# Kernel tuning notes

Hardware: AMD Instinct MI355X
Metric: run time of the kernel (lower is better)

Reference implementation:

```python
import jax, jax.numpy as jnp
import numpy as np


def _resize_axis(x, axis, n_out):
    # trilinear (per-axis linear) resize, matching torch align_corners=False
    n_in = x.shape[axis]
    coords = jnp.clip((jnp.arange(n_out) + 0.5) * (n_in / n_out) - 0.5, 0.0, n_in - 1)
    lo = jnp.floor(coords).astype(jnp.int32)
    hi = jnp.minimum(lo + 1, n_in - 1)
    w = (coords - lo).astype(x.dtype)
    shp = [1] * x.ndim
    shp[axis] = n_out
    w = w.reshape(shp)
    return jnp.take(x, lo, axis=axis) * (1 - w) + jnp.take(x, hi, axis=axis) * w


def setup_inputs() -> dict:
    key = jax.random.key(0)
    ks = jax.random.split(key, 16)
    M, B, C, H, W, Z = 4, 1, 64, 64, 64, 64
    mini = max(C // 32, 4)  # = 4
    s = 0.05
    return {
        'modalities': jax.random.normal(ks[0], (M, B, C, H, W, Z), jnp.float32),
        'wq1': jax.random.normal(ks[1], (mini, C), jnp.float32) * s,
        'bq1': jax.random.normal(ks[2], (mini,), jnp.float32) * s,
        'wq2': jax.random.normal(ks[3], (2, mini), jnp.float32) * s,
        'bq2': jax.random.normal(ks[4], (2,), jnp.float32) * s,
        'wa1': jax.random.normal(ks[5], (mini, C), jnp.float32) * s,
        'ba1': jax.random.normal(ks[6], (mini,), jnp.float32) * s,
        'wa2': jax.random.normal(ks[7], (1, mini), jnp.float32) * s,
        'ba2': jax.random.normal(ks[8], (1,), jnp.float32) * s,
        'wf': jax.random.normal(ks[9], (C, C), jnp.float32) * s,
        'bf': jax.random.normal(ks[10], (C,), jnp.float32) * s,
        'wg1': jax.random.normal(ks[11], (mini, C), jnp.float32) * s,
        'bg1': jax.random.normal(ks[12], (mini,), jnp.float32) * s,
        'wg2': jax.random.normal(ks[13], (C, mini), jnp.float32) * s,
        'bg2': jax.random.normal(ks[14], (C,), jnp.float32) * s,
    }


def reference(modalities, wq1, bq1, wq2, bq2, wa1, ba1, wa2, ba2, wf, bf, wg1, bg1, wg2, bg2):
    M, B, C, H, W, Z = modalities.shape
    x = modalities
    # quality net: GAP -> 1x1 conv -> relu -> 1x1 conv -> sigmoid (all 1x1x1 convs == matmuls)
    gap = x.mean(axis=(3, 4, 5))  # [M,B,C]
    scores = jax.nn.sigmoid(jnp.maximum(gap @ wq1.T + bq1, 0.0) @ wq2.T + bq2)  # [M,B,2]
    qw = scores.mean(axis=2)      # quality_weight per modality, [M,B] (mean over ch+unit spatial)
    t = qw.mean(axis=1)           # scalar weight contribution per modality, [M]
    # cross attention: adaptive avg pool to 4^3, tiny MLP, trilinear upsample back to H,W,Z
    d = x.reshape(M, B, C, 4, H // 4, 4, W // 4, 4, Z // 4).mean(axis=(4, 6, 8))  # [M,B,C,4,4,4]
    h = jnp.maximum(jnp.einsum('mbcxyz,kc->mbkxyz', d, wa1) + ba1.reshape(1, 1, -1, 1, 1, 1), 0.0)
    a = jax.nn.sigmoid(jnp.einsum('mbkxyz,ok->mboxyz', h, wa2) + ba2.reshape(1, 1, -1, 1, 1, 1))
    a = _resize_axis(_resize_axis(_resize_axis(a, 3, H), 4, W), 5, Z)  # [M,B,1,H,W,Z]
    # pairwise aggregation: enhancement_i = sum_{j!=i} x_j * attn_j * qw_j, normalized by sum_{j!=i} t_j
    contrib = x * a * qw[:, :, None, None, None, None]  # [M,B,C,H,W,Z]
    S = contrib.sum(axis=0, keepdims=True)
    T = t.sum()
    enh = (S - contrib) / (T - t)[:, None, None, None, None, None]
    # fusion 1x1 conv + gate
    fused = jnp.einsum('mbchwz,dc->mbdhwz', enh, wf) + bf.reshape(1, 1, -1, 1, 1, 1)
    g = fused.mean(axis=(3, 4, 5))  # [M,B,C]
    gate = jax.nn.sigmoid(jnp.maximum(g @ wg1.T + bg1, 0.0) @ wg2.T + bg2)  # [M,B,C]
    enhanced = x + gate[:, :, :, None, None, None] * fused
    boundary = scores[:, :, 0].reshape(M, B, 1, 1, 1, 1)
    semantic = scores[:, :, 1].reshape(M, B, 1, 1, 1, 1)
    return enhanced, boundary, semantic
```

## Files before the change

### kernel.cpp

```cpp
#include <hip/hip_runtime.h>
#include <math.h>

typedef __attribute__((ext_vector_type(4))) float f4;
typedef __attribute__((ext_vector_type(8))) short s8v;
typedef __attribute__((ext_vector_type(4))) unsigned int u4v;
typedef __attribute__((ext_vector_type(2))) unsigned int u2v;

#define NVOX 262144
#define MB_TOT 67108864

__device__ __forceinline__ float sigm(float x){ return 1.0f/(1.0f+expf(-x)); }
__device__ __forceinline__ unsigned short f2b(float f){
  unsigned x = __float_as_uint(f);
  return (unsigned short)((x + 0x7fffu + ((x>>16)&1u)) >> 16);
}
__device__ __forceinline__ unsigned cvtpk(float lo, float hi){
  unsigned r;
  asm("v_cvt_pk_bf16_f32 %0, %1, %2" : "=v"(r) : "v"(lo), "v"(hi));
  return r;
}
__device__ __forceinline__ float bl(unsigned u){ return __uint_as_float(u<<16); }
__device__ __forceinline__ float bh(unsigned u){ return __uint_as_float(u & 0xffff0000u); }

__global__ __launch_bounds__(1024) void k_pass1(const float* __restrict__ x,
                                                float* __restrict__ dsums,
                                                float* __restrict__ xbsums){
  __shared__ float rowdat[8][1024];
  __shared__ float txb[64][16];
  __shared__ float tbs[64][16];
  int tid = threadIdx.x;
  int mc = blockIdx.x;
  const float* xp = x + (size_t)mc * NVOX;
  int chunk = tid & 15;
  int rbase = tid >> 4;
  float wq0,wq1,wq2,wq3; int lzc;
  {
    int z0 = chunk*4;
    float cz = fminf(fmaxf((z0+0.5f)*0.0625f-0.5f, 0.0f), 3.0f);
    lzc = (int)cz;
    wq0 = cz - (float)lzc;
    cz = fminf(fmaxf((z0+1.5f)*0.0625f-0.5f, 0.0f), 3.0f); wq1 = cz - (float)lzc;
    cz = fminf(fmaxf((z0+2.5f)*0.0625f-0.5f, 0.0f), 3.0f); wq2 = cz - (float)lzc;
    cz = fminf(fmaxf((z0+3.5f)*0.0625f-0.5f, 0.0f), 3.0f); wq3 = cz - (float)lzc;
  }
  int kb = chunk >> 2;
  for (int round=0; round<4; ++round){
#pragma unroll
    for (int itg=0; itg<4; ++itg){
      f4 u[4];
#pragma unroll
      for (int s=0;s<4;++s){
        int it = itg*4+s;
        int row = round*1024 + it*64 + rbase;
        u[s] = *reinterpret_cast<const f4*>(xp + (size_t)row*64 + chunk*4);
      }
#pragma unroll
      for (int s=0;s<4;++s){
        int it = itg*4+s;
        int rir = it*64 + rbase;
        f4 v = u[s];
        float ksP = (v.x+v.y)+(v.z+v.w);
        float wB = v.x*wq0 + v.y*wq1 + v.z*wq2 + v.w*wq3;
        float wA = ksP - wB;
        ksP += __shfl_xor(ksP, 1, 64);
        ksP += __shfl_xor(ksP, 2, 64);
        float w0 = (lzc==0)?wA:0.f;
        float w1 = (lzc==1)?wA:((lzc==0)?wB:0.f);
        float w2 = (lzc==2)?wA:((lzc==1)?wB:0.f);
        float w3 = (lzc==3)?wA:((lzc==2)?wB:0.f);
#pragma unroll
        for (int mk=1; mk<16; mk<<=1){
          w0 += __shfl_xor(w0, mk, 64);
          w1 += __shfl_xor(w1, mk, 64);
          w2 += __shfl_xor(w2, mk, 64);
          w3 += __shfl_xor(w3, mk, 64);
        }
        if ((chunk&3)==0) rowdat[kb][rir] = ksP;
        if (chunk==0) rowdat[4][rir]=w0;
        if (chunk==1) rowdat[5][rir]=w1;
        if (chunk==2) rowdat[6][rir]=w2;
        if (chunk==3) rowdat[7][rir]=w3;
      }
    }
    __syncthreads();
    if (tid < 256){
      int il = tid>>4, py=(tid>>2)&3, pz=tid&3;
      int base = il*64;
      float s=0.f;
      for (int jj=0; jj<64; ++jj){
        int j = (jj + tid) & 63;
        float cj = fminf(fmaxf((j+0.5f)*0.0625f-0.5f, 0.0f), 3.0f);
        int lj=(int)cj; float wj=cj-(float)lj;
        float w = (py==lj)?(1.f-wj):((py==lj+1)?wj:0.f);
        s += w * rowdat[4+pz][base+j];
      }
      txb[round*16+il][py*4+pz] = s;
    } else if (tid < 512){
      int u2 = tid-256;
      int il = u2>>4, jq=(u2>>2)&3, kq=u2&3;
      int base = il*64 + jq*16;
      float s=0.f;
      for (int jj=0; jj<16; ++jj) s += rowdat[kq][base + ((jj+u2)&15)];
      tbs[round*16+il][jq*4+kq] = s;
    }
    __syncthreads();
  }
  if (tid < 64){
    int px = tid>>4, py=(tid>>2)&3, pz=tid&3;
    float s=0.f;
    for (int i=0;i<64;++i){
      float ci = fminf(fmaxf((i+0.5f)*0.0625f-0.5f, 0.0f), 3.0f);
      int li=(int)ci; float wi=ci-(float)li;
      float w = (px==li)?(1.f-wi):((px==li+1)?wi:0.f);
      s += w * txb[i][py*4+pz];
    }
    xbsums[(size_t)mc*64+tid] = s;
  } else if (tid < 128){
    int p = tid-64;
    int iq = p>>4, jq=(p>>2)&3, kq=p&3;
    float s=0.f;
    for (int i=iq*16; i<iq*16+16; ++i) s += tbs[i][jq*4+kq];
    dsums[(size_t)mc*64+p] = s;
  }
}

__global__ __launch_bounds__(256) void k_pass2(
    const float* __restrict__ dsums, const float* __restrict__ xbsums,
    const float* __restrict__ wq1, const float* __restrict__ bq1,
    const float* __restrict__ wq2, const float* __restrict__ bq2,
    const float* __restrict__ wa1, const float* __restrict__ ba1,
    const float* __restrict__ wa2, const float* __restrict__ ba2,
    const float* __restrict__ wf,  const float* __restrict__ bfv,
    const float* __restrict__ wg1, const float* __restrict__ bg1,
    const float* __restrict__ wg2, const float* __restrict__ bg2,
    float* __restrict__ wsa, float* __restrict__ wsgate,
    float* __restrict__ wsqw, float* __restrict__ wsinv,
    unsigned short* __restrict__ wfb,
    float* __restrict__ outp)
{
  __shared__ float sGap[256];
  __shared__ float sA[256];
  __shared__ float sCm[256];
  __shared__ float sG[256];
  __shared__ float sGG[16];
  __shared__ float sQw[4];
  int tid = threadIdx.x;
  int m = tid>>6, c = tid&63;
  for (int t = tid; t < 4096; t += 256) wfb[t] = f2b(wf[t]);
  {
    float s=0.f;
    const float* dp = dsums + (size_t)tid*64;
    for (int p=0;p<64;++p) s += dp[p];
    sGap[tid] = s * (1.0f/262144.0f);
  }
  {
    int p = c;
    float h0=0,h1=0,h2=0,h3=0;
    for (int cc=0; cc<64; ++cc){
      float dm = dsums[((size_t)(m*64+cc))*64+p] * (1.0f/4096.0f);
      h0 += dm * wa1[0*64+cc];
      h1 += dm * wa1[1*64+cc];
      h2 += dm * wa1[2*64+cc];
      h3 += dm * wa1[3*64+cc];
    }
    h0 = fmaxf(h0 + ba1[0], 0.f);
    h1 = fmaxf(h1 + ba1[1], 0.f);
    h2 = fmaxf(h2 + ba1[2], 0.f);
    h3 = fmaxf(h3 + ba1[3], 0.f);
    float s = h0*wa2[0] + h1*wa2[1] + h2*wa2[2] + h3*wa2[3] + ba2[0];
    float aa = sigm(s);
    sA[tid] = aa;
    wsa[tid] = aa;
  }
  __syncthreads();
  if (tid < 4){
    int mm = tid;
    float q0=0,q1=0,q2=0,q3=0;
    for (int cc=0; cc<64; ++cc){
      float g = sGap[mm*64+cc];
      q0 += g*wq1[0*64+cc];
      q1 += g*wq1[1*64+cc];
      q2 += g*wq1[2*64+cc];
      q3 += g*wq1[3*64+cc];
    }
    q0 = fmaxf(q0+bq1[0],0.f); q1 = fmaxf(q1+bq1[1],0.f);
    q2 = fmaxf(q2+bq1[2],0.f); q3 = fmaxf(q3+bq1[3],0.f);
    float s0 = sigm(q0*wq2[0]+q1*wq2[1]+q2*wq2[2]+q3*wq2[3]+bq2[0]);
    float s1 = sigm(q0*wq2[4]+q1*wq2[5]+q2*wq2[6]+q3*wq2[7]+bq2[1]);
    sQw[mm] = 0.5f*(s0+s1);
    outp[MB_TOT + mm]     = s0;
    outp[MB_TOT + 4 + mm] = s1;
  }
  __syncthreads();
  float qw_m = sQw[m];
  float T = sQw[0]+sQw[1]+sQw[2]+sQw[3];
  float inv_m = 1.0f/(T - qw_m);
  if (tid < 4){ wsqw[tid] = sQw[tid]; wsinv[tid] = 1.0f/(T - sQw[tid]); }
  {
    const float* xbp = xbsums + (size_t)tid*64;
    float s=0.f;
    for (int p=0;p<64;++p) s += sA[m*64+p]*xbp[p];
    sCm[tid] = qw_m * s * (1.0f/262144.0f);
  }
  __syncthreads();
  {
    int dd = c;
    float acc=0.f;
    for (int cc=0; cc<64; ++cc){
      float Sm = sCm[0*64+cc]+sCm[1*64+cc]+sCm[2*64+cc]+sCm[3*64+cc];
      float em = (Sm - sCm[m*64+cc]) * inv_m;
      acc += em * wf[dd*64+cc];
    }
    sG[tid] = acc + bfv[dd];
  }
  __syncthreads();
  if (tid < 16){
    int mm = tid>>2, k = tid&3;
    float acc=0.f;
    for (int dd=0; dd<64; ++dd) acc += sG[mm*64+dd]*wg1[k*64+dd];
    sGG[tid] = fmaxf(acc + bg1[k], 0.f);
  }
  __syncthreads();
  {
    float s = sGG[m*4+0]*wg2[c*4+0] + sGG[m*4+1]*wg2[c*4+1]
            + sGG[m*4+2]*wg2[c*4+2] + sGG[m*4+3]*wg2[c*4+3] + bg2[c];
    wsgate[tid] = sigm(s);
  }
}

__global__ __launch_bounds__(256) void k_pass3(
    const float* __restrict__ x, const unsigned short* __restrict__ wfb,
    const float* __restrict__ bfv,
    const float* __restrict__ wsa, const float* __restrict__ wsgate,
    const float* __restrict__ wsqw, const float* __restrict__ wsinv,
    float* __restrict__ outp)
{
  __shared__ unsigned int xt[4][32][66];
  __shared__ unsigned int fusedT[64][34];
  __shared__ float aCell[4][64];
  __shared__ float gateL[4][64];
  __shared__ __align__(16) float auq[4][64];
  __shared__ float bfL[64];
  __shared__ float A2[4][4];
  int tid = threadIdx.x;
  int b = blockIdx.x;
  int i = b >> 6, j = b & 63;
  size_t V0 = (size_t)b * 64;
  int w    = tid >> 6;
  int lane = tid & 63;
  int ks   = lane >> 4;
  int r    = lane & 15;
  int vox16 = w << 4;

  const float* xw = x + (size_t)(w*64)*NVOX + V0 + r*4;
  f4 v[16];
#pragma unroll
  for (int rr=0; rr<16; ++rr){
    int cc = ks*16 + rr;
    v[rr] = *reinterpret_cast<const f4*>(xw + (size_t)cc*NVOX);
  }
  aCell[w][lane] = wsa[tid];
  gateL[w][lane] = wsgate[tid];
  if (tid < 64) bfL[tid] = bfv[tid];
#pragma unroll
  for (int rr=0; rr<16; rr+=2){
    u4v pk;
#pragma unroll
    for (int q=0;q<4;++q) pk[q] = cvtpk(v[rr][q], v[rr+1][q]);
    *reinterpret_cast<u4v*>(&xt[w][ks*8 + (rr>>1)][r*4]) = pk;
  }
  __syncthreads();

  if (tid < 16){
    int mm = tid>>2, pz = tid&3;
    float ci = fminf(fmaxf((i+0.5f)*0.0625f-0.5f,0.f),3.f);
    int li=(int)ci; float wi=ci-(float)li; int hiI=li<3?li+1:3;
    float cj = fminf(fmaxf((j+0.5f)*0.0625f-0.5f,0.f),3.f);
    int lj=(int)cj; float wj=cj-(float)lj; int hj=lj<3?lj+1:3;
    A2[mm][pz] = (1.f-wi)*((1.f-wj)*aCell[mm][li*16+lj*4+pz] + wj*aCell[mm][li*16+hj*4+pz])
               + wi*((1.f-wj)*aCell[mm][hiI*16+lj*4+pz] + wj*aCell[mm][hiI*16+hj*4+pz]);
  }
  __syncthreads();
  {
    int mm = tid>>6, z = tid&63;
    float cz = fminf(fmaxf((z+0.5f)*0.0625f-0.5f,0.f),3.f);
    int lz=(int)cz; float wzf=cz-(float)lz; int hz=lz<3?lz+1:3;
    auq[mm][z] = ((1.f-wzf)*A2[mm][lz] + wzf*A2[mm][hz]) * wsqw[mm];
  }
  __syncthreads();

  s8v bfr[4][2];
#pragma unroll
  for (int t=0;t<4;++t)
#pragma unroll
    for (int kk=0;kk<2;++kk)
      bfr[t][kk] = *reinterpret_cast<const s8v*>(&wfb[(t*16 + r)*64 + kk*32 + ks*8]);

  f4 acc[4][4];
#pragma unroll
  for (int mm=0;mm<4;++mm)
#pragma unroll
    for (int t=0;t<4;++t) acc[mm][t] = f4{0.f,0.f,0.f,0.f};

#pragma unroll
  for (int mm=0;mm<4;++mm){
    union { unsigned int u[4]; s8v s; } A0, A1;
#pragma unroll
    for (int q=0;q<4;++q){
      A0.u[q] = xt[mm][ks*4+q][vox16+r];
      A1.u[q] = xt[mm][16+ks*4+q][vox16+r];
    }
#pragma unroll
    for (int t=0;t<4;++t){
      acc[mm][t] = __builtin_amdgcn_mfma_f32_16x16x32_bf16(A0.s, bfr[t][0], acc[mm][t], 0,0,0);
      acc[mm][t] = __builtin_amdgcn_mfma_f32_16x16x32_bf16(A1.s, bfr[t][1], acc[mm][t], 0,0,0);
    }
  }

  f4 aq[4]; float invv[4];
#pragma unroll
  for (int mm=0;mm<4;++mm){
    aq[mm]  = *reinterpret_cast<const f4*>(&auq[mm][vox16 + 4*ks]);
    invv[mm] = wsinv[mm];
  }
  f4 FS[4];
#pragma unroll
  for (int t=0;t<4;++t){
    FS[t] = f4{0.f,0.f,0.f,0.f};
#pragma unroll
    for (int mm=0;mm<4;++mm)
#pragma unroll
      for (int q=0;q<4;++q) FS[t][q] += aq[mm][q]*acc[mm][t][q];
  }

  int g4 = tid >> 4;
  int r4l = tid & 15;
#pragma unroll
  for (int mm=0;mm<4;++mm){
#pragma unroll
    for (int t=0;t<4;++t){
      int dd = t*16 + r;
      float bfvv = bfL[dd];
      float f0 = (FS[t][0] - aq[mm][0]*acc[mm][t][0])*invv[mm] + bfvv;
      float f1 = (FS[t][1] - aq[mm][1]*acc[mm][t][1])*invv[mm] + bfvv;
      float f2 = (FS[t][2] - aq[mm][2]*acc[mm][t][2])*invv[mm] + bfvv;
      float f3 = (FS[t][3] - aq[mm][3]*acc[mm][t][3])*invv[mm] + bfvv;
      u2v pk2;
      pk2.x = cvtpk(f0, f1);
      pk2.y = cvtpk(f2, f3);
      *reinterpret_cast<u2v*>(&fusedT[dd][(vox16 + ks*4)>>1]) = pk2;
    }
    __syncthreads();
#pragma unroll
    for (int rr=0; rr<4; ++rr){
      int dd = rr*16 + g4;
      float g = gateL[mm][dd];
      u4v xu = *reinterpret_cast<const u4v*>(&xt[mm][dd>>1][r4l*4]);
      u2v fu = *reinterpret_cast<const u2v*>(&fusedT[dd][r4l*2]);
      f4 o;
      float x0 = (dd&1) ? bh(xu[0]) : bl(xu[0]);
      float x1 = (dd&1) ? bh(xu[1]) : bl(xu[1]);
      float x2 = (dd&1) ? bh(xu[2]) : bl(xu[2]);
      float x3 = (dd&1) ? bh(xu[3]) : bl(xu[3]);
      o[0] = x0 + g*bl(fu.x);
      o[1] = x1 + g*bh(fu.x);
      o[2] = x2 + g*bl(fu.y);
      o[3] = x3 + g*bh(fu.y);
      *reinterpret_cast<f4*>(outp + (size_t)(mm*64+dd)*NVOX + V0 + r4l*4) = o;
    }
    __syncthreads();
  }
}

extern "C" void kernel_launch(void* const* d_in, const int* in_sizes, int n_in,
                              void* d_out, int out_size, void* d_ws, size_t ws_size,
                              hipStream_t stream){
  const float* x   = (const float*)d_in[0];
  const float* wq1 = (const float*)d_in[1];
  const float* bq1 = (const float*)d_in[2];
  const float* wq2 = (const float*)d_in[3];
  const float* bq2 = (const float*)d_in[4];
  const float* wa1 = (const float*)d_in[5];
  const float* ba1 = (const float*)d_in[6];
  const float* wa2 = (const float*)d_in[7];
  const float* ba2 = (const float*)d_in[8];
  const float* wf  = (const float*)d_in[9];
  const float* bfv = (const float*)d_in[10];
  const float* wg1 = (const float*)d_in[11];
  const float* bg1 = (const float*)d_in[12];
  const float* wg2 = (const float*)d_in[13];
  const float* bg2 = (const float*)d_in[14];
  float* outp = (float*)d_out;
  float* w = (float*)d_ws;
  float* dsums  = w;
  float* xbsums = w + 16384;
  float* wsa    = w + 32768;
  float* wsgate = w + 33024;
  float* wsqw   = w + 33280;
  float* wsinv  = w + 33284;
  unsigned short* wfb = (unsigned short*)(w + 33288);
  hipLaunchKernelGGL(k_pass1, dim3(256), dim3(1024), 0, stream, x, dsums, xbsums);
  hipLaunchKernelGGL(k_pass2, dim3(1), dim3(256), 0, stream, dsums, xbsums,
                     wq1,bq1,wq2,bq2,wa1,ba1,wa2,ba2,wf,bfv,wg1,bg1,wg2,bg2,
                     wsa, wsgate, wsqw, wsinv, wfb, outp);
  hipLaunchKernelGGL(k_pass3, dim3(4096), dim3(256), 0, stream, x, wfb, bfv,
                     wsa, wsgate, wsqw, wsinv, outp);
}
```

Baseline: 212.8 us.

## Restructure pass1 reduction into per-thread register accumulators with LDS atomics

Rewrites the first-pass reduction so each thread owns one (j, z-chunk) column and walks all 64 i rows, accumulating the downsampled sums and the trilinear-weighted sums in registers. A few LDS atomics per thread then replace the staged row buffers, the wide shuffle reductions and the multiple sync rounds. It also pads the transposed LDS tile in pass3 and reverses that kernel's block order, probably to get L2 reuse from data pass1 just read. Trade-offs are higher register pressure from the fully unrolled 64-iteration loop, and atomic contention on the 64 shared bins.

```diff
diff --git a/kernel.cpp b/kernel.cpp
--- a/kernel.cpp
+++ b/kernel.cpp
@@ -22,105 +22,76 @@
 __device__ __forceinline__ float bl(unsigned u){ return __uint_as_float(u<<16); }
 __device__ __forceinline__ float bh(unsigned u){ return __uint_as_float(u & 0xffff0000u); }
 
-__global__ __launch_bounds__(1024) void k_pass1(const float* __restrict__ x,
-                                                float* __restrict__ dsums,
-                                                float* __restrict__ xbsums){
-  __shared__ float rowdat[8][1024];
-  __shared__ float txb[64][16];
-  __shared__ float tbs[64][16];
+__global__ __launch_bounds__(1024, 4) void k_pass1(const float* __restrict__ x,
+                                                   float* __restrict__ dsums,
+                                                   float* __restrict__ xbsums){
+  __shared__ float xbL[64];
+  __shared__ float bsL[64];
   int tid = threadIdx.x;
   int mc = blockIdx.x;
+  if (tid < 64){ xbL[tid]=0.f; bsL[tid]=0.f; }
   const float* xp = x + (size_t)mc * NVOX;
   int chunk = tid & 15;
-  int rbase = tid >> 4;
-  float wq0,wq1,wq2,wq3; int lzc;
-  {
-    int z0 = chunk*4;
-    float cz = fminf(fmaxf((z0+0.5f)*0.0625f-0.5f, 0.0f), 3.0f);
-    lzc = (int)cz;
-    wq0 = cz - (float)lzc;
-    cz = fminf(fmaxf((z0+1.5f)*0.0625f-0.5f, 0.0f), 3.0f); wq1 = cz - (float)lzc;
-    cz = fminf(fmaxf((z0+2.5f)*0.0625f-0.5f, 0.0f), 3.0f); wq2 = cz - (float)lzc;
-    cz = fminf(fmaxf((z0+3.5f)*0.0625f-0.5f, 0.0f), 3.0f); wq3 = cz - (float)lzc;
-  }
-  int kb = chunk >> 2;
-  for (int round=0; round<4; ++round){
-#pragma unroll
-    for (int itg=0; itg<4; ++itg){
-      f4 u[4];
-#pragma unroll
-      for (int s=0;s<4;++s){
-        int it = itg*4+s;
-        int row = round*1024 + it*64 + rbase;
-        u[s] = *reinterpret_cast<const f4*>(xp + (size_t)row*64 + chunk*4);
-      }
-#pragma unroll
-      for (int s=0;s<4;++s){
-        int it = itg*4+s;
-        int rir = it*64 + rbase;
-        f4 v = u[s];
-        float ksP = (v.x+v.y)+(v.z+v.w);
-        float wB = v.x*wq0 + v.y*wq1 + v.z*wq2 + v.w*wq3;
-        float wA = ksP - wB;
-        ksP += __shfl_xor(ksP, 1, 64);
-        ksP += __shfl_xor(ksP, 2, 64);
-        float w0 = (lzc==0)?wA:0.f;
-        float w1 = (lzc==1)?wA:((lzc==0)?wB:0.f);
-        float w2 = (lzc==2)?wA:((lzc==1)?wB:0.f);
-        float w3 = (lzc==3)?wA:((lzc==2)?wB:0.f);
-#pragma unroll
-        for (int mk=1; mk<16; mk<<=1){
-          w0 += __shfl_xor(w0, mk, 64);
-          w1 += __shfl_xor(w1, mk, 64);
-          w2 += __shfl_xor(w2, mk, 64);
-          w3 += __shfl_xor(w3, mk, 64);
-        }
-        if ((chunk&3)==0) rowdat[kb][rir] = ksP;
-        if (chunk==0) rowdat[4][rir]=w0;
-        if (chunk==1) rowdat[5][rir]=w1;
-        if (chunk==2) rowdat[6][rir]=w2;
-        if (chunk==3) rowdat[7][rir]=w3;
-      }
-    }
-    __syncthreads();
-    if (tid < 256){
-      int il = tid>>4, py=(tid>>2)&3, pz=tid&3;
-      int base = il*64;
-      float s=0.f;
-      for (int jj=0; jj<64; ++jj){
-        int j = (jj + tid) & 63;
-        float cj = fminf(fmaxf((j+0.5f)*0.0625f-0.5f, 0.0f), 3.0f);
-        int lj=(int)cj; float wj=cj-(float)lj;
-        float w = (py==lj)?(1.f-wj):((py==lj+1)?wj:0.f);
-        s += w * rowdat[4+pz][base+j];
-      }
-      txb[round*16+il][py*4+pz] = s;
-    } else if (tid < 512){
-      int u2 = tid-256;
-      int il = u2>>4, jq=(u2>>2)&3, kq=u2&3;
-      int base = il*64 + jq*16;
-      float s=0.f;
-      for (int jj=0; jj<16; ++jj) s += rowdat[kq][base + ((jj+u2)&15)];
-      tbs[round*16+il][jq*4+kq] = s;
-    }
-    __syncthreads();
-  }
+  int j     = tid >> 4;
+  float wqz0,wqz1,wqz2,wqz3; int lzc;
+  {
+    float cz = fminf(fmaxf((chunk*4+0.5f)*0.0625f-0.5f, 0.0f), 3.0f);
+    lzc = (int)cz;  wqz0 = cz - (float)lzc;
+    cz = fminf(fmaxf((chunk*4+1.5f)*0.0625f-0.5f, 0.0f), 3.0f); wqz1 = cz - (float)lzc;
+    cz = fminf(fmaxf((chunk*4+2.5f)*0.0625f-0.5f, 0.0f), 3.0f); wqz2 = cz - (float)lzc;
+    cz = fminf(fmaxf((chunk*4+3.5f)*0.0625f-0.5f, 0.0f), 3.0f); wqz3 = cz - (float)lzc;
+  }
+  float cjA, cjB; int lj;
+  {
+    float cj = fminf(fmaxf((j+0.5f)*0.0625f-0.5f, 0.0f), 3.0f);
+    lj = (int)cj; float wj = cj - (float)lj;
+    cjA = 1.0f - wj; cjB = wj;
+  }
+  int jq = j >> 4, kq = chunk >> 2;
+
+  float accx[4][2][2];
+#pragma unroll
+  for (int a=0;a<4;++a){ accx[a][0][0]=0.f; accx[a][0][1]=0.f; accx[a][1][0]=0.f; accx[a][1][1]=0.f; }
+  float accb0=0.f, accb1=0.f, accb2=0.f, accb3=0.f;
+
+#pragma unroll
+  for (int i=0; i<64; ++i){
+    f4 v = *reinterpret_cast<const f4*>(xp + (size_t)(i*64 + j)*64 + chunk*4);
+    float s  = (v.x+v.y)+(v.z+v.w);
+    float wB = v.x*wqz0 + v.y*wqz1 + v.z*wqz2 + v.w*wqz3;
+    float wA = s - wB;
+    if ((i>>4)==0) accb0 += s; else if ((i>>4)==1) accb1 += s;
+    else if ((i>>4)==2) accb2 += s; else accb3 += s;
+    float ci = fminf(fmaxf((i+0.5f)*0.0625f-0.5f, 0.0f), 3.0f);
+    int li = (int)ci; float wi = ci - (float)li;
+    {
+      float pA = 1.0f - wi;
+      float e0 = pA*wA, e1 = pA*wB;
+      accx[li][0][0] += cjA*e0;  accx[li][0][1] += cjA*e1;
+      accx[li][1][0] += cjB*e0;  accx[li][1][1] += cjB*e1;
+    }
+    if (wi > 0.0f){
+      float f0 = wi*wA, f1 = wi*wB;
+      accx[li+1][0][0] += cjA*f0;  accx[li+1][0][1] += cjA*f1;
+      accx[li+1][1][0] += cjB*f0;  accx[li+1][1][1] += cjB*f1;
+    }
+  }
+  __syncthreads();
+#pragma unroll
+  for (int px=0; px<4; ++px){
+    atomicAdd(&xbL[px*16 + lj*4 + lzc], accx[px][0][0]);
+    if (lzc < 3) atomicAdd(&xbL[px*16 + lj*4 + lzc+1], accx[px][0][1]);
+    if (lj  < 3) atomicAdd(&xbL[px*16 + (lj+1)*4 + lzc], accx[px][1][0]);
+    if (lj < 3 && lzc < 3) atomicAdd(&xbL[px*16 + (lj+1)*4 + lzc+1], accx[px][1][1]);
+  }
+  atomicAdd(&bsL[0*16 + jq*4 + kq], accb0);
+  atomicAdd(&bsL[1*16 + jq*4 + kq], accb1);
+  atomicAdd(&bsL[2*16 + jq*4 + kq], accb2);
+  atomicAdd(&bsL[3*16 + jq*4 + kq], accb3);
+  __syncthreads();
   if (tid < 64){
-    int px = tid>>4, py=(tid>>2)&3, pz=tid&3;
-    float s=0.f;
-    for (int i=0;i<64;++i){
-      float ci = fminf(fmaxf((i+0.5f)*0.0625f-0.5f, 0.0f), 3.0f);
-      int li=(int)ci; float wi=ci-(float)li;
-      float w = (px==li)?(1.f-wi):((px==li+1)?wi:0.f);
-      s += w * txb[i][py*4+pz];
-    }
-    xbsums[(size_t)mc*64+tid] = s;
-  } else if (tid < 128){
-    int p = tid-64;
-    int iq = p>>4, jq=(p>>2)&3, kq=p&3;
-    float s=0.f;
-    for (int i=iq*16; i<iq*16+16; ++i) s += tbs[i][jq*4+kq];
-    dsums[(size_t)mc*64+p] = s;
+    xbsums[(size_t)mc*64 + tid] = xbL[tid];
+    dsums [(size_t)mc*64 + tid] = bsL[tid];
   }
 }
 
@@ -235,7 +206,7 @@
     const float* __restrict__ wsqw, const float* __restrict__ wsinv,
     float* __restrict__ outp)
 {
-  __shared__ unsigned int xt[4][32][66];
+  __shared__ unsigned int xt[4][32][68];
   __shared__ unsigned int fusedT[64][34];
   __shared__ float aCell[4][64];
   __shared__ float gateL[4][64];
@@ -243,7 +214,7 @@
   __shared__ float bfL[64];
   __shared__ float A2[4][4];
   int tid = threadIdx.x;
-  int b = blockIdx.x;
+  int b = 4095 - (int)blockIdx.x;
   int i = b >> 6, j = b & 63;
   size_t V0 = (size_t)b * 64;
   int w    = tid >> 6;
```

Result: slower. 299.3 us (+40.6%).

## Split pass1 blocks in half with atomic accumulation and reverse pass3 block order

Applied to the files above, without the earlier changes.

Pass1 now launches two blocks per (modality, channel), each covering half the rows, and accumulates partial pooled sums into workspace with atomicAdd after a memset clears it. This doubles the block count so the 256-CU GPU is better filled during the bandwidth-bound reduction. Pass3 walks its blocks in reverse order, probably so data pass1 touched last is still in cache when pass3 starts, and pads the xt shared array. The cost is an extra memset launch and atomics, and floating-point summation order is no longer deterministic.

```diff
diff --git a/kernel.cpp b/kernel.cpp
--- a/kernel.cpp
+++ b/kernel.cpp
@@ -26,25 +26,26 @@
                                                 float* __restrict__ dsums,
                                                 float* __restrict__ xbsums){
   __shared__ float rowdat[8][1024];
-  __shared__ float txb[64][16];
-  __shared__ float tbs[64][16];
+  __shared__ float txb[32][16];
+  __shared__ float tbs[32][16];
   int tid = threadIdx.x;
-  int mc = blockIdx.x;
+  int b = blockIdx.x;
+  int mc   = b >> 1;
+  int half = b & 1;
   const float* xp = x + (size_t)mc * NVOX;
   int chunk = tid & 15;
   int rbase = tid >> 4;
   float wq0,wq1,wq2,wq3; int lzc;
   {
-    int z0 = chunk*4;
-    float cz = fminf(fmaxf((z0+0.5f)*0.0625f-0.5f, 0.0f), 3.0f);
-    lzc = (int)cz;
-    wq0 = cz - (float)lzc;
-    cz = fminf(fmaxf((z0+1.5f)*0.0625f-0.5f, 0.0f), 3.0f); wq1 = cz - (float)lzc;
-    cz = fminf(fmaxf((z0+2.5f)*0.0625f-0.5f, 0.0f), 3.0f); wq2 = cz - (float)lzc;
-    cz = fminf(fmaxf((z0+3.5f)*0.0625f-0.5f, 0.0f), 3.0f); wq3 = cz - (float)lzc;
+    float cz = fminf(fmaxf((chunk*4+0.5f)*0.0625f-0.5f, 0.0f), 3.0f);
+    lzc = (int)cz;  wq0 = cz - (float)lzc;
+    cz = fminf(fmaxf((chunk*4+1.5f)*0.0625f-0.5f, 0.0f), 3.0f); wq1 = cz - (float)lzc;
+    cz = fminf(fmaxf((chunk*4+2.5f)*0.0625f-0.5f, 0.0f), 3.0f); wq2 = cz - (float)lzc;
+    cz = fminf(fmaxf((chunk*4+3.5f)*0.0625f-0.5f, 0.0f), 3.0f); wq3 = cz - (float)lzc;
   }
   int kb = chunk >> 2;
-  for (int round=0; round<4; ++round){
+  for (int r2=0; r2<2; ++r2){
+    int round = half*2 + r2;
 #pragma unroll
     for (int itg=0; itg<4; ++itg){
       f4 u[4];
@@ -52,7 +53,7 @@
       for (int s=0;s<4;++s){
         int it = itg*4+s;
         int row = round*1024 + it*64 + rbase;
-        u[s] = *reinterpret_cast<const f4*>(xp + (size_t)row*64 + chunk*4);
+        u[s] = *reinterpret_cast<const f4*>(xp + (size_t)row * 64 + chunk*4);
       }
 #pragma unroll
       for (int s=0;s<4;++s){
@@ -94,33 +95,34 @@
         float w = (py==lj)?(1.f-wj):((py==lj+1)?wj:0.f);
         s += w * rowdat[4+pz][base+j];
       }
-      txb[round*16+il][py*4+pz] = s;
+      txb[r2*16+il][py*4+pz] = s;
     } else if (tid < 512){
       int u2 = tid-256;
       int il = u2>>4, jq=(u2>>2)&3, kq=u2&3;
       int base = il*64 + jq*16;
       float s=0.f;
       for (int jj=0; jj<16; ++jj) s += rowdat[kq][base + ((jj+u2)&15)];
-      tbs[round*16+il][jq*4+kq] = s;
+      tbs[r2*16+il][jq*4+kq] = s;
     }
     __syncthreads();
   }
   if (tid < 64){
     int px = tid>>4, py=(tid>>2)&3, pz=tid&3;
     float s=0.f;
-    for (int i=0;i<64;++i){
+    for (int il=0; il<32; ++il){
+      int i = half*32 + il;
       float ci = fminf(fmaxf((i+0.5f)*0.0625f-0.5f, 0.0f), 3.0f);
       int li=(int)ci; float wi=ci-(float)li;
       float w = (px==li)?(1.f-wi):((px==li+1)?wi:0.f);
-      s += w * txb[i][py*4+pz];
-    }
-    xbsums[(size_t)mc*64+tid] = s;
-  } else if (tid < 128){
-    int p = tid-64;
-    int iq = p>>4, jq=(p>>2)&3, kq=p&3;
+      s += w * txb[il][py*4+pz];
+    }
+    atomicAdd(&xbsums[(size_t)mc*64+tid], s);
+  } else if (tid < 96){
+    int p_loc = tid-64;
+    int iq_loc = p_loc>>4, inner = p_loc&15;
     float s=0.f;
-    for (int i=iq*16; i<iq*16+16; ++i) s += tbs[i][jq*4+kq];
-    dsums[(size_t)mc*64+p] = s;
+    for (int il=iq_loc*16; il<iq_loc*16+16; ++il) s += tbs[il][inner];
+    atomicAdd(&dsums[(size_t)mc*64 + (half*2+iq_loc)*16 + inner], s);
   }
 }
 
@@ -235,7 +237,7 @@
     const float* __restrict__ wsqw, const float* __restrict__ wsinv,
     float* __restrict__ outp)
 {
-  __shared__ unsigned int xt[4][32][66];
+  __shared__ unsigned int xt[4][32][68];
   __shared__ unsigned int fusedT[64][34];
   __shared__ float aCell[4][64];
   __shared__ float gateL[4][64];
@@ -243,7 +245,7 @@
   __shared__ float bfL[64];
   __shared__ float A2[4][4];
   int tid = threadIdx.x;
-  int b = blockIdx.x;
+  int b = 4095 - (int)blockIdx.x;
   int i = b >> 6, j = b & 63;
   size_t V0 = (size_t)b * 64;
   int w    = tid >> 6;
@@ -399,7 +401,8 @@
   float* wsqw   = w + 33280;
   float* wsinv  = w + 33284;
   unsigned short* wfb = (unsigned short*)(w + 33288);
-  hipLaunchKernelGGL(k_pass1, dim3(256), dim3(1024), 0, stream, x, dsums, xbsums);
+  hipMemsetAsync(w, 0, 32768*sizeof(float), stream);
+  hipLaunchKernelGGL(k_pass1, dim3(512), dim3(1024), 0, stream, x, dsums, xbsums);
   hipLaunchKernelGGL(k_pass2, dim3(1), dim3(256), 0, stream, dsums, xbsums,
                      wq1,bq1,wq2,bq2,wa1,ba1,wa2,ba2,wf,bfv,wg1,bg1,wg2,bg2,
                      wsa, wsgate, wsqw, wsinv, wfb, outp);
```

New measurement: 197.6 us, median of 2. 1.08x faster.
